# Kernel tuning notes

Hardware: AMD Instinct MI355X
Metric: run time of the kernel (lower is better)

## Reference

```python
import jax, jax.numpy as jnp
import numpy as np

NUM_GROUPS = 512
GROUP_SIZE = 32
GROUP_RADIUS = 0.2
K_ORIGINAL = 5 * GROUP_SIZE  # ball_query oversampling factor from the source


def setup_inputs() -> dict:
    key = jax.random.key(0)
    k1, k2 = jax.random.split(key)
    B, N, C = 8, 16384, 4
    points = jax.random.normal(k1, (B, N, C), dtype=jnp.float32)
    # valid lengths in [N//2, N) so the lengths-masking path is exercised
    lengths = (N // 2 + jax.random.randint(k2, (B,), 0, N // 2)).astype(jnp.int32)
    return {"points": points, "lengths": lengths}


def _sample_farthest_points(xyz, lengths, K):
    # xyz: (B,N,3) float, lengths: (B,) int -> centers (B,K,3)
    B, N, _ = xyz.shape
    n_idx = jnp.arange(N)

    def per_batch(pts, length):
        valid = n_idx < length

        def step(carry, _):
            mindist, cur = carry
            d = jnp.sum((pts - pts[cur]) ** 2, axis=-1)  # (N,)
            mindist = jnp.where(valid, jnp.minimum(mindist, d), -jnp.inf)
            nxt = jnp.argmax(mindist).astype(jnp.int32)
            return (mindist, nxt), cur

        mindist0 = jnp.where(valid, jnp.inf, -jnp.inf)
        # deterministic start at index 0 (source uses random_start_point=True)
        (_, _), sel = jax.lax.scan(step, (mindist0, jnp.int32(0)), None, length=K)
        return pts[sel]

    return jax.vmap(per_batch)(xyz, lengths)


def _ball_query(centers, xyz, lengths, K, radius):
    # returns first-K (by point index, matching pytorch3d ball_query) indices
    # within radius; -1 padding. centers (B,G,3), xyz (B,N,3) -> idx (B,G,K)
    B, G, _ = centers.shape
    N = xyz.shape[1]
    d2 = jnp.sum((centers[:, :, None, :] - xyz[:, None, :, :]) ** 2, axis=-1)  # (B,G,N)
    valid = (jnp.arange(N) < lengths[:, None])[:, None, :]  # (B,1,N)
    mask = (d2 < radius * radius) & valid
    # score N-n > 0 iff in ball; top_k picks smallest indices first (in order)
    score = jnp.where(mask, N - jnp.arange(N, dtype=jnp.int32), jnp.int32(-1))
    vals, _ = jax.lax.top_k(score, K)
    return jnp.where(vals > 0, N - vals, -1)  # (B,G,K)


def _select_topk_by_energy(points, idx, K_new):
    # points (B,N,C), idx (B,G,K_orig) with -1 invalid -> (B,G,K_new)
    B, G, _ = idx.shape
    N = points.shape[1]
    invalid = idx == -1
    idxc = jnp.maximum(idx, 0)
    energies = jnp.broadcast_to(points[:, None, :, 3], (B, G, N))
    e = jnp.take_along_axis(energies, idxc, axis=2)  # (B,G,K_orig)
    e = jnp.where(invalid, -jnp.inf, e)
    top_e, top_i = jax.lax.top_k(e, K_new)
    topk_idx = jnp.take_along_axis(idx, top_i, axis=2)
    return jnp.where(top_e == -jnp.inf, -1, topk_idx)


def _masked_gather(points, idx):
    # points (B,N,C), idx (B,G,K); -1 -> gathered value 0.0 (pytorch3d semantics)
    B, G, K = idx.shape
    C = points.shape[-1]
    valid = idx >= 0
    flat = jnp.maximum(idx, 0).reshape(B, G * K)
    g = jnp.take_along_axis(points, flat[:, :, None], axis=1).reshape(B, G, K, C)
    return jnp.where(valid[..., None], g, 0.0)


def _forward(points, lengths):
    xyz = points[:, :, :3]
    centers = _sample_farthest_points(xyz, lengths, NUM_GROUPS)  # (B,G,3)
    idx = _ball_query(centers, xyz, lengths, K_ORIGINAL, GROUP_RADIUS)
    idx = _select_topk_by_energy(points, idx, GROUP_SIZE)  # (B,G,K)
    # fill_empty_indices: replace -1 with first index of the group
    first = idx[:, :, :1]
    idx = jnp.where(idx == -1, first, idx)
    groups = _masked_gather(points, idx)  # (B,G,K,C)
    groups = jnp.concatenate(
        [groups[..., :3] - centers[:, :, None, :], groups[..., 3:]], axis=-1
    )
    groups = groups / GROUP_RADIUS
    return groups, centers


def reference(points, lengths):
    return _forward(points, lengths)
```

## Files before the change

### kernel.cpp

```cpp
#include <hip/hip_runtime.h>

constexpr int B_ = 8;
constexpr int N_ = 16384;
constexpr int NG = 512;
constexpr int GS = 32;
constexpr int KORIG = 160;
constexpr int TPB = 1024;
constexpr int PPT = 16;
#define R2 0.04f
#define RADIUS 0.2f

__device__ __forceinline__ unsigned f32_ord(float f) {
  unsigned u = __float_as_uint(f);
  return (u & 0x80000000u) ? ~u : (u | 0x80000000u);
}

template <int CTRL>
__device__ __forceinline__ float dpp_fmax(float v) {
  int o = __builtin_amdgcn_update_dpp(0, __float_as_int(v), CTRL, 0xF, 0xF, true);
  return fmaxf(v, __int_as_float(o));
}
__device__ __forceinline__ float wave_fmax(float v) {
  v = dpp_fmax<0xB1>(v);
  v = dpp_fmax<0x4E>(v);
  v = dpp_fmax<0x141>(v);
  v = dpp_fmax<0x140>(v);
  v = fmaxf(v, __int_as_float(__builtin_amdgcn_ds_swizzle(__float_as_int(v), 0x401F)));
  v = fmaxf(v, __shfl_xor(v, 32, 64));
  return v;
}
__device__ __forceinline__ float group16_fmax(float v) {
  v = dpp_fmax<0xB1>(v);
  v = dpp_fmax<0x4E>(v);
  v = dpp_fmax<0x141>(v);
  v = dpp_fmax<0x140>(v);
  return v;
}

__global__ __launch_bounds__(1024, 4) void fps_kernel(const float4* __restrict__ p4,
                                                      const int* __restrict__ lengths,
                                                      float* __restrict__ centers) {
#pragma clang fp contract(off)
  const int b = blockIdx.x;
  const int t = threadIdx.x;
  const int lane = t & 63;
  const int wid = t >> 6;
  const int len = lengths[b];
  const float4* bp = p4 + (size_t)b * N_;

  __shared__ float2 sxy[N_];
  __shared__ float pubf[16];
  __shared__ float4 cpub;

  const int mybase = wid * 1024 + lane;

  float z[PPT], m[PPT];
#pragma unroll
  for (int j = 0; j < PPT; ++j) {
    const int i = t * PPT + j;
    float4 p = bp[i];
    sxy[mybase + j * 64] = make_float2(p.x, p.y);
    z[j] = p.z;
    m[j] = (i < len) ? __builtin_inff() : -__builtin_inff();
  }
  __syncthreads();

  float4 c0 = bp[0];
  float cx = c0.x, cy = c0.y, cz = c0.z;
  if (t == 0) {
    size_t o = (size_t)b * NG * 3;
    centers[o] = cx; centers[o + 1] = cy; centers[o + 2] = cz;
  }

  for (int k = 0; k < NG - 1; ++k) {
#pragma unroll
    for (int j = 0; j < PPT; ++j) {
      float2 xy = sxy[mybase + j * 64];
      float dx = xy.x - cx;
      float dy = xy.y - cy;
      float dz = z[j] - cz;
      float d = dx * dx + dy * dy + dz * dz;
      m[j] = fminf(m[j], d);
    }
    float u0 = fmaxf(m[0], m[1]),   u1 = fmaxf(m[2], m[3]);
    float u2 = fmaxf(m[4], m[5]),   u3 = fmaxf(m[6], m[7]);
    float u4 = fmaxf(m[8], m[9]),   u5 = fmaxf(m[10], m[11]);
    float u6 = fmaxf(m[12], m[13]), u7 = fmaxf(m[14], m[15]);
    float v0 = fmaxf(u0, u1), v1 = fmaxf(u2, u3);
    float v2 = fmaxf(u4, u5), v3 = fmaxf(u6, u7);
    const float sm = fmaxf(fmaxf(v0, v1), fmaxf(v2, v3));

    const float wmax = wave_fmax(sm);
    if (lane == 0) pubf[wid] = wmax;
    __syncthreads();

    const float pw = pubf[lane & 15];
    const float kmax = group16_fmax(pw);
    const unsigned long long bal = __ballot(pw == kmax);
    const int grp = lane & 48;
    const int ww = __ffsll((bal >> grp) & 0xFFFFull) - 1;

    if (wid == ww) {
      int jsel = 0;
      float zs = z[0];
      bool fnd = (m[0] == kmax);
#pragma unroll
      for (int j = 1; j < PPT; ++j) {
        const bool sel = (m[j] == kmax) && !fnd;
        jsel = sel ? j : jsel;
        zs = sel ? z[j] : zs;
        fnd = fnd || sel;
      }
      const unsigned long long mb = __ballot(fnd);
      const int wl = __ffsll(mb) - 1;
      if (lane == wl) {
        float2 xy = sxy[mybase + jsel * 64];
        cpub = make_float4(xy.x, xy.y, zs, 0.0f);
      }
    }
    __syncthreads();

    const float4 c = cpub;
    cx = c.x; cy = c.y; cz = c.z;
    if (t == 0) {
      size_t o = ((size_t)b * NG + (k + 1)) * 3;
      centers[o] = cx; centers[o + 1] = cy; centers[o + 2] = cz;
    }
  }
}

__global__ __launch_bounds__(64) void group_kernel(const float4* __restrict__ p4,
                                                   const int* __restrict__ lengths,
                                                   const float* __restrict__ centers,
                                                   float4* __restrict__ outg) {
#pragma clang fp contract(off)
  const int gid = blockIdx.x;
  const int b = gid >> 9;
  const int lane = threadIdx.x;
  const int len = lengths[b];
  const float4* bp = p4 + (size_t)b * N_;
  const float cx = centers[(size_t)gid * 3 + 0];
  const float cy = centers[(size_t)gid * 3 + 1];
  const float cz = centers[(size_t)gid * 3 + 2];

  __shared__ int cand[KORIG];
  int M = 0;
  for (int cb = 0; cb < N_ && M < KORIG; cb += 256) {
#pragma unroll
    for (int q = 0; q < 4; ++q) {
      const int i = cb + q * 64 + lane;
      float4 p = bp[i];
      float dx = p.x - cx;
      float dy = p.y - cy;
      float dz = p.z - cz;
      float d2 = dx * dx + dy * dy + dz * dz;
      const bool pred = (i < len) && (d2 < R2);
      unsigned long long mb = __ballot(pred);
      if (pred) {
        int pos = M + (int)__popcll(mb & ((1ull << lane) - 1ull));
        if (pos < KORIG) cand[pos] = i;
      }
      M += (int)__popcll(mb);
    }
  }
  if (M > KORIG) M = KORIG;
  __syncthreads();

  const unsigned long long SENT = ~0ull;
  unsigned long long key0 = SENT, key1 = SENT, key2 = SENT;
  {
    int c0 = lane, c1 = lane + 64, c2 = lane + 128;
    if (c0 < M) { int i = cand[c0]; key0 = ((unsigned long long)(~f32_ord(bp[i].w)) << 32) | (unsigned)i; }
    if (c1 < M) { int i = cand[c1]; key1 = ((unsigned long long)(~f32_ord(bp[i].w)) << 32) | (unsigned)i; }
    if (c2 < M) { int i = cand[c2]; key2 = ((unsigned long long)(~f32_ord(bp[i].w)) << 32) | (unsigned)i; }
  }

  int mysel = -1;
  for (int j = 0; j < GS; ++j) {
    unsigned long long kmin = key0 < key1 ? key0 : key1;
    if (key2 < kmin) kmin = key2;
#pragma unroll
    for (int off = 32; off > 0; off >>= 1) {
      unsigned long long o = __shfl_xor(kmin, off, 64);
      if (o < kmin) kmin = o;
    }
    if (kmin == SENT) break;
    if (lane == j) mysel = (int)(unsigned)kmin;
    if (key0 == kmin) key0 = SENT;
    if (key1 == kmin) key1 = SENT;
    if (key2 == kmin) key2 = SENT;
  }

  const int first = __shfl(mysel, 0, 64);
  if (lane < GS) {
    int idx = (mysel < 0) ? first : mysel;
    float4 o;
    if (idx >= 0) {
      float4 p = bp[idx];
      o.x = (p.x - cx) / RADIUS;
      o.y = (p.y - cy) / RADIUS;
      o.z = (p.z - cz) / RADIUS;
      o.w = p.w / RADIUS;
    } else {
      o.x = (0.0f - cx) / RADIUS;
      o.y = (0.0f - cy) / RADIUS;
      o.z = (0.0f - cz) / RADIUS;
      o.w = 0.0f;
    }
    outg[(size_t)gid * GS + lane] = o;
  }
}

extern "C" void kernel_launch(void* const* d_in, const int* in_sizes, int n_in,
                              void* d_out, int out_size, void* d_ws, size_t ws_size,
                              hipStream_t stream) {
  const float4* pts = (const float4*)d_in[0];
  const int* lengths = (const int*)d_in[1];
  float* out = (float*)d_out;
  float* centers = out + (size_t)B_ * NG * GS * 4;
  float4* groups = (float4*)out;

  fps_kernel<<<B_, TPB, 0, stream>>>(pts, lengths, centers);
  group_kernel<<<B_ * NG, 64, 0, stream>>>(pts, lengths, centers, groups);
}
```

Before: 974.3 us.

## Publish per-wave argmax index to drop second barrier in FPS loop

Each thread now finds which of its 16 points holds its local maximum with a branchless tournament. The wave's winning lane publishes that point index next to the max value, in double-buffered shared arrays. After the single barrier, every wave reads the winning index and loads the next center straight from global memory. This removes the second __syncthreads and the serial selection pass on each of the 511 iterations. In exchange, each iteration now pays a dependent global (cache-hit) load latency.

Result: faster. 906.1 us (-7.0%).

```diff
diff --git a/kernel.cpp b/kernel.cpp
--- a/kernel.cpp
+++ b/kernel.cpp
@@ -49,8 +49,8 @@
   const float4* bp = p4 + (size_t)b * N_;
 
   __shared__ float2 sxy[N_];
-  __shared__ float pubf[16];
-  __shared__ float4 cpub;
+  __shared__ float pubf[2][16];
+  __shared__ int pubi[2][16];
 
   const int mybase = wid * 1024 + lane;
 
@@ -88,40 +88,41 @@
     float u6 = fmaxf(m[12], m[13]), u7 = fmaxf(m[14], m[15]);
     float v0 = fmaxf(u0, u1), v1 = fmaxf(u2, u3);
     float v2 = fmaxf(u4, u5), v3 = fmaxf(u6, u7);
-    const float sm = fmaxf(fmaxf(v0, v1), fmaxf(v2, v3));
+    float w0 = fmaxf(v0, v1), w1 = fmaxf(v2, v3);
+    const float sm = fmaxf(w0, w1);
+
+    const bool b3 = (w0 != sm);
+    const float vL = b3 ? v2 : v0;
+    const bool b2 = (vL != sm);
+    const float uL = b3 ? (b2 ? u6 : u4) : (b2 ? u2 : u0);
+    const bool b1 = (uL != sm);
+    const int hi3 = ((int)b3 << 3) | ((int)b2 << 2) | ((int)b1 << 1);
+    const float mL = (hi3 & 8) ? ((hi3 & 4) ? ((hi3 & 2) ? m[14] : m[12])
+                                            : ((hi3 & 2) ? m[10] : m[8]))
+                               : ((hi3 & 4) ? ((hi3 & 2) ? m[6] : m[4])
+                                            : ((hi3 & 2) ? m[2] : m[0]));
+    const bool b0 = (mL != sm);
+    const int bj = hi3 | (int)b0;
 
     const float wmax = wave_fmax(sm);
-    if (lane == 0) pubf[wid] = wmax;
+    const unsigned long long att = __ballot(sm == wmax);
+    const int wl = __ffsll(att) - 1;
+    if (lane == wl) {
+      pubf[k & 1][wid] = wmax;
+      pubi[k & 1][wid] = t * PPT + bj;
+    }
     __syncthreads();
 
-    const float pw = pubf[lane & 15];
+    const float pw = pubf[k & 1][lane & 15];
     const float kmax = group16_fmax(pw);
     const unsigned long long bal = __ballot(pw == kmax);
     const int grp = lane & 48;
     const int ww = __ffsll((bal >> grp) & 0xFFFFull) - 1;
-
-    if (wid == ww) {
-      int jsel = 0;
-      float zs = z[0];
-      bool fnd = (m[0] == kmax);
-#pragma unroll
-      for (int j = 1; j < PPT; ++j) {
-        const bool sel = (m[j] == kmax) && !fnd;
-        jsel = sel ? j : jsel;
-        zs = sel ? z[j] : zs;
-        fnd = fnd || sel;
-      }
-      const unsigned long long mb = __ballot(fnd);
-      const int wl = __ffsll(mb) - 1;
-      if (lane == wl) {
-        float2 xy = sxy[mybase + jsel * 64];
-        cpub = make_float4(xy.x, xy.y, zs, 0.0f);
-      }
-    }
-    __syncthreads();
-
-    const float4 c = cpub;
+    const int nxt = pubi[k & 1][ww];
+    const int snxt = __builtin_amdgcn_readfirstlane(nxt);
+    const float4 c = bp[snxt];
     cx = c.x; cy = c.y; cz = c.z;
+
     if (t == 0) {
       size_t o = ((size_t)b * NG + (k + 1)) * 3;
       centers[o] = cx; centers[o + 1] = cy; centers[o + 2] = cz;
```
